# Performance work log

Hardware: AMD Instinct MI355X
Metric: run time of the kernel (lower is better)

## Reference

```python
import jax, jax.numpy as jnp
import numpy as np

FP16_MIN = -65504.0
FP16_MAX = 65504.0

B, S, D, H = 2, 2048, 1024, 16
HD = D // H


def setup_inputs() -> dict:
    key = jax.random.key(0)
    ks = jax.random.split(key, 12)
    s = 0.02
    inp = {
        "x_q": jax.random.normal(ks[0], (B, S, D), jnp.float32),
        "x_k": jax.random.normal(ks[1], (B, S, D), jnp.float32),
        "x_v": jax.random.normal(ks[2], (B, S, D), jnp.float32),
        # causal mask [B, 1, S, S]; 0 entries are masked out
        "mask": jnp.broadcast_to(jnp.tril(jnp.ones((S, S), jnp.int32)), (B, 1, S, S)),
        "Wq": jax.random.normal(ks[3], (D, D), jnp.float32) * s,
        "bq": jnp.zeros((D,), jnp.float32),
        "Wk": jax.random.normal(ks[4], (D, D), jnp.float32) * s,
        "bk": jnp.zeros((D,), jnp.float32),
        "Wv": jax.random.normal(ks[5], (D, D), jnp.float32) * s,
        "bv": jnp.zeros((D,), jnp.float32),
        "Wo": jax.random.normal(ks[6], (D, D), jnp.float32) * s,
        "bo": jnp.zeros((D,), jnp.float32),
    }
    return inp


def _split_heads(x):
    # [B, S, D] -> [B, H, S, HD]
    b, s, _ = x.shape
    return x.reshape(b, s, H, HD).transpose(0, 2, 1, 3)


def reference(x_q, x_k, x_v, mask, Wq, bq, Wk, bk, Wv, bv, Wo, bo):
    scale = jnp.sqrt(jnp.float32(HD))
    q = _split_heads(x_q @ Wq + bq)  # [B,H,S,HD]
    k = _split_heads(x_k @ Wk + bk)
    v = _split_heads(x_v @ Wv + bv)

    scores = jnp.einsum("bhqd,bhkd->bhqk", q, k) / scale  # [B,H,S,S]
    scores = jnp.where(mask == 0, FP16_MIN, scores)
    scores = jnp.where(jnp.isneginf(scores), FP16_MIN, scores)
    scores = jnp.where(jnp.isposinf(scores), FP16_MAX, scores)

    probs = jax.nn.softmax(scores, axis=-1)  # dropout p=0.0 -> identity
    ctx = jnp.einsum("bhqk,bhkd->bhqd", probs, v)  # [B,H,S,HD]
    ctx = ctx.transpose(0, 2, 1, 3).reshape(x_q.shape[0], x_q.shape[1], D)
    out = ctx @ Wo + bo
    return out, probs
```

## Files before the change

kernel.cpp:

```cpp
#include <hip/hip_runtime.h>


typedef __bf16 bf16x8 __attribute__((ext_vector_type(8)));
typedef float f32x4 __attribute__((ext_vector_type(4)));

__device__ __forceinline__ unsigned short f2bf(float f) {
  unsigned int u = __builtin_bit_cast(unsigned int, f);
  u += 0x7fffu + ((u >> 16) & 1u);
  return (unsigned short)(u >> 16);
}
__device__ __forceinline__ float bf2f_lo(unsigned int u) {
  return __builtin_bit_cast(float, u << 16);
}
__device__ __forceinline__ float bf2f_hi(unsigned int u) {
  return __builtin_bit_cast(float, u & 0xffff0000u);
}

__global__ void transpose_w(const float* __restrict__ W0, const float* __restrict__ W1,
                            const float* __restrict__ W2, const float* __restrict__ W3,
                            unsigned short* __restrict__ Wt) {
  __shared__ float t[32][33];
  const int z = blockIdx.z;
  const float* W = (z == 0) ? W0 : (z == 1) ? W1 : (z == 2) ? W2 : W3;
  unsigned short* o = Wt + (size_t)z * 1048576u;
  const int n0 = blockIdx.x * 32, k0 = blockIdx.y * 32;
  const int tx = threadIdx.x, ty = threadIdx.y;
#pragma unroll
  for (int i = 0; i < 4; i++)
    t[ty + 8 * i][tx] = W[(size_t)(k0 + ty + 8 * i) * 1024 + n0 + tx];
  __syncthreads();
#pragma unroll
  for (int i = 0; i < 4; i++)
    o[(size_t)(n0 + ty + 8 * i) * 1024 + k0 + tx] = f2bf(t[tx][ty + 8 * i]);
}

__global__ __launch_bounds__(256) void gemm_kernel(
    const void* __restrict__ A0, const void* __restrict__ A1, const void* __restrict__ A2,
    const unsigned short* __restrict__ Wtb,
    const float* __restrict__ b0, const float* __restrict__ b1, const float* __restrict__ b2,
    void* __restrict__ O0, void* __restrict__ O1, void* __restrict__ O2,
    const int mode0) {
  __shared__ unsigned short Alds[128 * 40];
  const int z = blockIdx.z;
  const int mode = mode0 + z;
  const void* Av = (z == 0) ? A0 : (z == 1) ? A1 : A2;
  const float* bias = (z == 0) ? b0 : (z == 1) ? b1 : b2;
  void* outv = (z == 0) ? O0 : (z == 1) ? O1 : O2;
  const unsigned short* Wt = Wtb + (size_t)z * 1048576u;

  const int tid = threadIdx.x;
  const int lane = tid & 63;
  const int wave = tid >> 6;
  const int wm = wave >> 1, wn = wave & 1;
  const int m0 = blockIdx.y * 128, n0 = blockIdx.x * 128;
  const int g = lane >> 4, c = lane & 15;

  f32x4 acc[4][4];
#pragma unroll
  for (int i = 0; i < 4; i++)
#pragma unroll
    for (int j = 0; j < 4; j++) acc[i][j] = (f32x4){0.f, 0.f, 0.f, 0.f};

  const int srow = tid >> 1;
  const int sch = (tid & 1) * 16;

  for (int kb = 0; kb < 1024; kb += 32) {
    if (mode < 3) {
      const float* A = (const float*)Av;
      const float4* src = (const float4*)(A + (size_t)(m0 + srow) * 1024 + kb + sch);
      unsigned int pk[8];
#pragma unroll
      for (int i = 0; i < 4; i++) {
        float4 v = src[i];
        pk[2 * i]     = (unsigned int)f2bf(v.x) | ((unsigned int)f2bf(v.y) << 16);
        pk[2 * i + 1] = (unsigned int)f2bf(v.z) | ((unsigned int)f2bf(v.w) << 16);
      }
      uint4* dst = (uint4*)&Alds[srow * 40 + sch];
      dst[0] = make_uint4(pk[0], pk[1], pk[2], pk[3]);
      dst[1] = make_uint4(pk[4], pk[5], pk[6], pk[7]);
    } else {
      const unsigned short* A = (const unsigned short*)Av;
      const uint4* src = (const uint4*)(A + (size_t)(m0 + srow) * 1024 + kb + sch);
      uint4* dst = (uint4*)&Alds[srow * 40 + sch];
      dst[0] = src[0];
      dst[1] = src[1];
    }
    __syncthreads();

    bf16x8 af[4], bfr[4];
#pragma unroll
    for (int mi = 0; mi < 4; mi++)
      af[mi] = *(const bf16x8*)&Alds[(wm * 64 + mi * 16 + c) * 40 + g * 8];
#pragma unroll
    for (int nf = 0; nf < 4; nf++)
      bfr[nf] = *(const bf16x8*)(Wt + (size_t)(n0 + wn * 64 + nf * 16 + c) * 1024 + kb + g * 8);
#pragma unroll
    for (int mi = 0; mi < 4; mi++)
#pragma unroll
      for (int nf = 0; nf < 4; nf++)
        acc[mi][nf] = __builtin_amdgcn_mfma_f32_16x16x32_bf16(af[mi], bfr[nf], acc[mi][nf], 0, 0, 0);
    __syncthreads();
  }

#pragma unroll
  for (int nf = 0; nf < 4; nf++) {
    const int col = n0 + wn * 64 + nf * 16 + c;
    const float bc = bias[col];
#pragma unroll
    for (int mi = 0; mi < 4; mi++) {
#pragma unroll
      for (int r = 0; r < 4; r++) {
        const int row = m0 + wm * 64 + mi * 16 + g * 4 + r;
        const float v = acc[mi][nf][r] + bc;
        if (mode == 0) {
          ((unsigned short*)outv)[(size_t)row * 1024 + col] = f2bf(v * 0.125f);
        } else if (mode == 1) {
          ((unsigned short*)outv)[(size_t)row * 1024 + col] = f2bf(v);
        } else if (mode == 2) {
          const int bb = row >> 11, s = row & 2047;
          ((unsigned short*)outv)[((size_t)(bb * 1024 + col)) * 2048 + s] = f2bf(v);
        } else {
          ((float*)outv)[(size_t)row * 1024 + col] = v;
        }
      }
    }
  }
}

__global__ __launch_bounds__(256) void attn_kernel(
    const unsigned short* __restrict__ Q, const unsigned short* __restrict__ K,
    const unsigned short* __restrict__ Vt, float* __restrict__ probs,
    unsigned short* __restrict__ ctx) {
  __shared__ unsigned short Klds[64 * 72];
  __shared__ unsigned short Vlds[64 * 72];
  __shared__ unsigned short Plds[64 * 72];

  const int tid = threadIdx.x;
  const int lane = tid & 63, wave = tid >> 6;
  const int g = lane >> 4, c = lane & 15;
  const int q0 = blockIdx.x * 64;
  const int h = blockIdx.y, b = blockIdx.z;
  const int qrow0 = q0 + wave * 16;

  const unsigned short* Qh = Q + ((size_t)(b * 2048 + qrow0)) * 1024 + h * 64;
  const unsigned short* Kh = K + ((size_t)b * 2048) * 1024 + h * 64;
  const unsigned short* Vh = Vt + ((size_t)(b * 16 + h)) * 64 * 2048;
  float* Ph = probs + ((size_t)((b * 16 + h) * 2048 + q0)) * 2048;

  const bf16x8 qa0 = *(const bf16x8*)&Qh[(size_t)c * 1024 + g * 8];
  const bf16x8 qa1 = *(const bf16x8*)&Qh[(size_t)c * 1024 + 32 + g * 8];

  const int srow = tid >> 2;
  const int scol = (tid & 3) * 16;
  const int kb_end = q0 + 64;

#define QK_TILE()                                                                        \
  f32x4 sv[4];                                                                           \
  _Pragma("unroll")                                                                      \
  for (int sub = 0; sub < 4; sub++) {                                                    \
    sv[sub] = (f32x4){0.f, 0.f, 0.f, 0.f};                                               \
    const unsigned short* Kr = &Klds[(sub * 16 + c) * 72];                               \
    sv[sub] = __builtin_amdgcn_mfma_f32_16x16x32_bf16(qa0, *(const bf16x8*)&Kr[g * 8], sv[sub], 0, 0, 0); \
    sv[sub] = __builtin_amdgcn_mfma_f32_16x16x32_bf16(qa1, *(const bf16x8*)&Kr[32 + g * 8], sv[sub], 0, 0, 0); \
  }                                                                                      \
  if (kb + 63 > qrow0) {                                                                 \
    _Pragma("unroll")                                                                    \
    for (int sub = 0; sub < 4; sub++)                                                    \
      _Pragma("unroll")                                                                  \
      for (int r = 0; r < 4; r++)                                                        \
        if (kb + sub * 16 + c > qrow0 + g * 4 + r) sv[sub][r] = -1e30f;                  \
  }

  float lp[4] = {0.f, 0.f, 0.f, 0.f};
  for (int kb = 0; kb < kb_end; kb += 64) {
    {
      const uint4* ksrc = (const uint4*)(Kh + (size_t)(kb + srow) * 1024 + scol);
      uint4* kdst = (uint4*)&Klds[srow * 72 + scol];
      kdst[0] = ksrc[0];
      kdst[1] = ksrc[1];
    }
    __syncthreads();
    QK_TILE();
#pragma unroll
    for (int r = 0; r < 4; r++)
      lp[r] += __expf(sv[0][r]) + __expf(sv[1][r]) + __expf(sv[2][r]) + __expf(sv[3][r]);
    __syncthreads();
  }
#pragma unroll
  for (int off = 1; off < 16; off <<= 1)
#pragma unroll
    for (int r = 0; r < 4; r++) lp[r] += __shfl_xor(lp[r], off);
  float invl[4];
#pragma unroll
  for (int r = 0; r < 4; r++) invl[r] = 1.0f / lp[r];

  f32x4 cacc[4];
#pragma unroll
  for (int nf = 0; nf < 4; nf++) cacc[nf] = (f32x4){0.f, 0.f, 0.f, 0.f};

  for (int kb = 0; kb < kb_end; kb += 64) {
    {
      const uint4* ksrc = (const uint4*)(Kh + (size_t)(kb + srow) * 1024 + scol);
      uint4* kdst = (uint4*)&Klds[srow * 72 + scol];
      kdst[0] = ksrc[0];
      kdst[1] = ksrc[1];
      const uint4* vsrc = (const uint4*)(Vh + (size_t)srow * 2048 + kb + scol);
      uint4* vdst = (uint4*)&Vlds[srow * 72 + scol];
      vdst[0] = vsrc[0];
      vdst[1] = vsrc[1];
    }
    __syncthreads();
    QK_TILE();
#pragma unroll
    for (int sub = 0; sub < 4; sub++)
#pragma unroll
      for (int r = 0; r < 4; r++) {
        const float p = __expf(sv[sub][r]) * invl[r];
        Plds[(wave * 16 + g * 4 + r) * 72 + sub * 16 + c] = f2bf(p);
      }
    const bf16x8 pa0 = *(const bf16x8*)&Plds[(wave * 16 + c) * 72 + g * 8];
    const bf16x8 pa1 = *(const bf16x8*)&Plds[(wave * 16 + c) * 72 + 32 + g * 8];
#pragma unroll
    for (int nf = 0; nf < 4; nf++) {
      const bf16x8 vf0 = *(const bf16x8*)&Vlds[(nf * 16 + c) * 72 + g * 8];
      const bf16x8 vf1 = *(const bf16x8*)&Vlds[(nf * 16 + c) * 72 + 32 + g * 8];
      cacc[nf] = __builtin_amdgcn_mfma_f32_16x16x32_bf16(pa0, vf0, cacc[nf], 0, 0, 0);
      cacc[nf] = __builtin_amdgcn_mfma_f32_16x16x32_bf16(pa1, vf1, cacc[nf], 0, 0, 0);
    }
    __syncthreads();
    {
      const int row = tid >> 2;
      const int cb = (tid & 3) * 16;
      const uint4* ps = (const uint4*)&Plds[row * 72 + cb];
      const uint4 a = ps[0], bb4 = ps[1];
      float* dst = Ph + (size_t)row * 2048 + kb + cb;
      ((float4*)dst)[0] = make_float4(bf2f_lo(a.x), bf2f_hi(a.x), bf2f_lo(a.y), bf2f_hi(a.y));
      ((float4*)dst)[1] = make_float4(bf2f_lo(a.z), bf2f_hi(a.z), bf2f_lo(a.w), bf2f_hi(a.w));
      ((float4*)dst)[2] = make_float4(bf2f_lo(bb4.x), bf2f_hi(bb4.x), bf2f_lo(bb4.y), bf2f_hi(bb4.y));
      ((float4*)dst)[3] = make_float4(bf2f_lo(bb4.z), bf2f_hi(bb4.z), bf2f_lo(bb4.w), bf2f_hi(bb4.w));
    }
  }
#undef QK_TILE

#pragma unroll
  for (int nf = 0; nf < 4; nf++)
#pragma unroll
    for (int r = 0; r < 4; r++)
      ctx[((size_t)(b * 2048 + qrow0 + g * 4 + r)) * 1024 + h * 64 + nf * 16 + c] =
          f2bf(cacc[nf][r]);

  if (kb_end < 2048) {
    const float4 zz = make_float4(0.f, 0.f, 0.f, 0.f);
    for (int row = 0; row < 64; ++row) {
      float* pr = Ph + (size_t)row * 2048;
      for (int col = kb_end + tid * 4; col < 2048; col += 1024)
        *(float4*)&pr[col] = zz;
    }
  }
}

extern "C" void kernel_launch(void* const* d_in, const int* in_sizes, int n_in,
                              void* d_out, int out_size, void* d_ws, size_t ws_size,
                              hipStream_t stream) {
  if (ws_size < (size_t)40 * 1024 * 1024) return;

  const float* xq = (const float*)d_in[0];
  const float* xk = (const float*)d_in[1];
  const float* xv = (const float*)d_in[2];
  const float* Wq = (const float*)d_in[4];
  const float* bq = (const float*)d_in[5];
  const float* Wk = (const float*)d_in[6];
  const float* bk = (const float*)d_in[7];
  const float* Wv = (const float*)d_in[8];
  const float* bv = (const float*)d_in[9];
  const float* Wo = (const float*)d_in[10];
  const float* bo = (const float*)d_in[11];

  unsigned short* ws = (unsigned short*)d_ws;
  unsigned short* Wt = ws;
  unsigned short* Qw = ws + (size_t)4 * 1048576u;
  unsigned short* Kw = Qw + 4194304u;
  unsigned short* Vtw = Kw + 4194304u;
  unsigned short* Cw = Vtw + 4194304u;

  float* out = (float*)d_out;
  float* probs = out + 4194304u;

  transpose_w<<<dim3(32, 32, 4), dim3(32, 8), 0, stream>>>(Wq, Wk, Wv, Wo, Wt);
  gemm_kernel<<<dim3(8, 32, 3), 256, 0, stream>>>(xq, xk, xv, Wt, bq, bk, bv,
                                                  Qw, Kw, Vtw, 0);
  attn_kernel<<<dim3(32, 16, 2), 256, 0, stream>>>(Qw, Kw, Vtw, probs, Cw);
  gemm_kernel<<<dim3(8, 32, 1), 256, 0, stream>>>(Cw, Cw, Cw, Wt + 3u * 1048576u,
                                                  bo, bo, bo, out, out, out, 3);
}
```

Before: 391.8 us.

## Halve GEMM M-tile with register prefetch; enlarge attention block to 128 queries

The GEMM now uses 64-row M tiles, so twice as many blocks are launched, and it prefetches the next K-slice of A into registers while the current slice is computed. The attention kernel moves to 512-thread blocks covering 128 query rows, which halves redundant K/V tile loads per query. It also register-prefetches the next K/V tiles, and waves past the causal diagonal skip compute and only write zero probabilities. In exchange, GEMM reuse of the weight reads drops and the attention blocks use more registers and LDS, which can reduce occupancy. The larger blocks also worsen load imbalance across the causal grid.

```diff
diff --git a/kernel.cpp b/kernel.cpp
--- a/kernel.cpp
+++ b/kernel.cpp
@@ -40,7 +40,7 @@
     const float* __restrict__ b0, const float* __restrict__ b1, const float* __restrict__ b2,
     void* __restrict__ O0, void* __restrict__ O1, void* __restrict__ O2,
     const int mode0) {
-  __shared__ unsigned short Alds[128 * 40];
+  __shared__ unsigned short Alds[64 * 40];
   const int z = blockIdx.z;
   const int mode = mode0 + z;
   const void* Av = (z == 0) ? A0 : (z == 1) ? A1 : A2;
@@ -52,65 +52,64 @@
   const int lane = tid & 63;
   const int wave = tid >> 6;
   const int wm = wave >> 1, wn = wave & 1;
-  const int m0 = blockIdx.y * 128, n0 = blockIdx.x * 128;
+  const int m0 = blockIdx.y * 64, n0 = blockIdx.x * 128;
   const int g = lane >> 4, c = lane & 15;
 
-  f32x4 acc[4][4];
-#pragma unroll
-  for (int i = 0; i < 4; i++)
+  f32x4 acc[2][4];
+#pragma unroll
+  for (int i = 0; i < 2; i++)
 #pragma unroll
     for (int j = 0; j < 4; j++) acc[i][j] = (f32x4){0.f, 0.f, 0.f, 0.f};
 
-  const int srow = tid >> 1;
-  const int sch = (tid & 1) * 16;
-
+  const int srow = tid >> 2;
+  const int sch = (tid & 3) * 8;
+
+#define LOAD_PACK(KB, DST)                                                        \
+  if (mode < 3) {                                                                 \
+    const float* A = (const float*)Av;                                            \
+    const float4* src = (const float4*)(A + (size_t)(m0 + srow) * 1024 + (KB) + sch); \
+    const float4 v0 = src[0], v1 = src[1];                                        \
+    DST.x = (unsigned int)f2bf(v0.x) | ((unsigned int)f2bf(v0.y) << 16);          \
+    DST.y = (unsigned int)f2bf(v0.z) | ((unsigned int)f2bf(v0.w) << 16);          \
+    DST.z = (unsigned int)f2bf(v1.x) | ((unsigned int)f2bf(v1.y) << 16);          \
+    DST.w = (unsigned int)f2bf(v1.z) | ((unsigned int)f2bf(v1.w) << 16);          \
+  } else {                                                                        \
+    const unsigned short* A = (const unsigned short*)Av;                          \
+    DST = *(const uint4*)(A + (size_t)(m0 + srow) * 1024 + (KB) + sch);           \
+  }
+
+  uint4 pk;
+  LOAD_PACK(0, pk);
   for (int kb = 0; kb < 1024; kb += 32) {
-    if (mode < 3) {
-      const float* A = (const float*)Av;
-      const float4* src = (const float4*)(A + (size_t)(m0 + srow) * 1024 + kb + sch);
-      unsigned int pk[8];
-#pragma unroll
-      for (int i = 0; i < 4; i++) {
-        float4 v = src[i];
-        pk[2 * i]     = (unsigned int)f2bf(v.x) | ((unsigned int)f2bf(v.y) << 16);
-        pk[2 * i + 1] = (unsigned int)f2bf(v.z) | ((unsigned int)f2bf(v.w) << 16);
-      }
-      uint4* dst = (uint4*)&Alds[srow * 40 + sch];
-      dst[0] = make_uint4(pk[0], pk[1], pk[2], pk[3]);
-      dst[1] = make_uint4(pk[4], pk[5], pk[6], pk[7]);
-    } else {
-      const unsigned short* A = (const unsigned short*)Av;
-      const uint4* src = (const uint4*)(A + (size_t)(m0 + srow) * 1024 + kb + sch);
-      uint4* dst = (uint4*)&Alds[srow * 40 + sch];
-      dst[0] = src[0];
-      dst[1] = src[1];
-    }
+    *(uint4*)&Alds[srow * 40 + sch] = pk;
+    if (kb + 32 < 1024) { LOAD_PACK(kb + 32, pk); }
     __syncthreads();
 
-    bf16x8 af[4], bfr[4];
-#pragma unroll
-    for (int mi = 0; mi < 4; mi++)
-      af[mi] = *(const bf16x8*)&Alds[(wm * 64 + mi * 16 + c) * 40 + g * 8];
+    bf16x8 af[2], bfr[4];
+#pragma unroll
+    for (int mi = 0; mi < 2; mi++)
+      af[mi] = *(const bf16x8*)&Alds[(wm * 32 + mi * 16 + c) * 40 + g * 8];
 #pragma unroll
     for (int nf = 0; nf < 4; nf++)
       bfr[nf] = *(const bf16x8*)(Wt + (size_t)(n0 + wn * 64 + nf * 16 + c) * 1024 + kb + g * 8);
 #pragma unroll
-    for (int mi = 0; mi < 4; mi++)
+    for (int mi = 0; mi < 2; mi++)
 #pragma unroll
       for (int nf = 0; nf < 4; nf++)
         acc[mi][nf] = __builtin_amdgcn_mfma_f32_16x16x32_bf16(af[mi], bfr[nf], acc[mi][nf], 0, 0, 0);
     __syncthreads();
   }
+#undef LOAD_PACK
 
 #pragma unroll
   for (int nf = 0; nf < 4; nf++) {
     const int col = n0 + wn * 64 + nf * 16 + c;
     const float bc = bias[col];
 #pragma unroll
-    for (int mi = 0; mi < 4; mi++) {
+    for (int mi = 0; mi < 2; mi++) {
 #pragma unroll
       for (int r = 0; r < 4; r++) {
-        const int row = m0 + wm * 64 + mi * 16 + g * 4 + r;
+        const int row = m0 + wm * 32 + mi * 16 + g * 4 + r;
         const float v = acc[mi][nf][r] + bc;
         if (mode == 0) {
           ((unsigned short*)outv)[(size_t)row * 1024 + col] = f2bf(v * 0.125f);
@@ -127,32 +126,34 @@
   }
 }
 
-__global__ __launch_bounds__(256) void attn_kernel(
+__global__ __launch_bounds__(512, 4) void attn_kernel(
     const unsigned short* __restrict__ Q, const unsigned short* __restrict__ K,
     const unsigned short* __restrict__ Vt, float* __restrict__ probs,
     unsigned short* __restrict__ ctx) {
   __shared__ unsigned short Klds[64 * 72];
   __shared__ unsigned short Vlds[64 * 72];
-  __shared__ unsigned short Plds[64 * 72];
+  __shared__ unsigned short Plds[128 * 72];
 
   const int tid = threadIdx.x;
   const int lane = tid & 63, wave = tid >> 6;
   const int g = lane >> 4, c = lane & 15;
-  const int q0 = blockIdx.x * 64;
-  const int h = blockIdx.y, b = blockIdx.z;
+  const int bh = blockIdx.x;
+  const int b = bh >> 4, h = bh & 15;
+  const int q0 = blockIdx.y * 128;
   const int qrow0 = q0 + wave * 16;
+  const int wave_kend = qrow0 + 16;
 
   const unsigned short* Qh = Q + ((size_t)(b * 2048 + qrow0)) * 1024 + h * 64;
   const unsigned short* Kh = K + ((size_t)b * 2048) * 1024 + h * 64;
-  const unsigned short* Vh = Vt + ((size_t)(b * 16 + h)) * 64 * 2048;
-  float* Ph = probs + ((size_t)((b * 16 + h) * 2048 + q0)) * 2048;
+  const unsigned short* Vh = Vt + ((size_t)bh) * 64 * 2048;
+  float* Ph = probs + ((size_t)(bh * 2048 + q0)) * 2048;
 
   const bf16x8 qa0 = *(const bf16x8*)&Qh[(size_t)c * 1024 + g * 8];
   const bf16x8 qa1 = *(const bf16x8*)&Qh[(size_t)c * 1024 + 32 + g * 8];
 
-  const int srow = tid >> 2;
-  const int scol = (tid & 3) * 16;
-  const int kb_end = q0 + 64;
+  const int srow = tid >> 3;
+  const int scol = (tid & 7) * 8;
+  const int kb_end = q0 + 128;
 
 #define QK_TILE()                                                                        \
   f32x4 sv[4];                                                                           \
@@ -172,19 +173,21 @@
   }
 
   float lp[4] = {0.f, 0.f, 0.f, 0.f};
-  for (int kb = 0; kb < kb_end; kb += 64) {
-    {
-      const uint4* ksrc = (const uint4*)(Kh + (size_t)(kb + srow) * 1024 + scol);
-      uint4* kdst = (uint4*)&Klds[srow * 72 + scol];
-      kdst[0] = ksrc[0];
-      kdst[1] = ksrc[1];
+  {
+    uint4 kreg = *(const uint4*)(Kh + (size_t)srow * 1024 + scol);
+    for (int kb = 0; kb < kb_end; kb += 64) {
+      *(uint4*)&Klds[srow * 72 + scol] = kreg;
+      if (kb + 64 < kb_end)
+        kreg = *(const uint4*)(Kh + (size_t)(kb + 64 + srow) * 1024 + scol);
+      __syncthreads();
+      if (kb < wave_kend) {
+        QK_TILE();
+#pragma unroll
+        for (int r = 0; r < 4; r++)
+          lp[r] += __expf(sv[0][r]) + __expf(sv[1][r]) + __expf(sv[2][r]) + __expf(sv[3][r]);
+      }
+      __syncthreads();
     }
-    __syncthreads();
-    QK_TILE();
-#pragma unroll
-    for (int r = 0; r < 4; r++)
-      lp[r] += __expf(sv[0][r]) + __expf(sv[1][r]) + __expf(sv[2][r]) + __expf(sv[3][r]);
-    __syncthreads();
   }
 #pragma unroll
   for (int off = 1; off < 16; off <<= 1)
@@ -198,46 +201,54 @@
 #pragma unroll
   for (int nf = 0; nf < 4; nf++) cacc[nf] = (f32x4){0.f, 0.f, 0.f, 0.f};
 
-  for (int kb = 0; kb < kb_end; kb += 64) {
-    {
-      const uint4* ksrc = (const uint4*)(Kh + (size_t)(kb + srow) * 1024 + scol);
-      uint4* kdst = (uint4*)&Klds[srow * 72 + scol];
-      kdst[0] = ksrc[0];
-      kdst[1] = ksrc[1];
-      const uint4* vsrc = (const uint4*)(Vh + (size_t)srow * 2048 + kb + scol);
-      uint4* vdst = (uint4*)&Vlds[srow * 72 + scol];
-      vdst[0] = vsrc[0];
-      vdst[1] = vsrc[1];
-    }
-    __syncthreads();
-    QK_TILE();
-#pragma unroll
-    for (int sub = 0; sub < 4; sub++)
-#pragma unroll
-      for (int r = 0; r < 4; r++) {
-        const float p = __expf(sv[sub][r]) * invl[r];
-        Plds[(wave * 16 + g * 4 + r) * 72 + sub * 16 + c] = f2bf(p);
-      }
-    const bf16x8 pa0 = *(const bf16x8*)&Plds[(wave * 16 + c) * 72 + g * 8];
-    const bf16x8 pa1 = *(const bf16x8*)&Plds[(wave * 16 + c) * 72 + 32 + g * 8];
-#pragma unroll
-    for (int nf = 0; nf < 4; nf++) {
-      const bf16x8 vf0 = *(const bf16x8*)&Vlds[(nf * 16 + c) * 72 + g * 8];
-      const bf16x8 vf1 = *(const bf16x8*)&Vlds[(nf * 16 + c) * 72 + 32 + g * 8];
-      cacc[nf] = __builtin_amdgcn_mfma_f32_16x16x32_bf16(pa0, vf0, cacc[nf], 0, 0, 0);
-      cacc[nf] = __builtin_amdgcn_mfma_f32_16x16x32_bf16(pa1, vf1, cacc[nf], 0, 0, 0);
-    }
-    __syncthreads();
-    {
-      const int row = tid >> 2;
-      const int cb = (tid & 3) * 16;
-      const uint4* ps = (const uint4*)&Plds[row * 72 + cb];
-      const uint4 a = ps[0], bb4 = ps[1];
-      float* dst = Ph + (size_t)row * 2048 + kb + cb;
-      ((float4*)dst)[0] = make_float4(bf2f_lo(a.x), bf2f_hi(a.x), bf2f_lo(a.y), bf2f_hi(a.y));
-      ((float4*)dst)[1] = make_float4(bf2f_lo(a.z), bf2f_hi(a.z), bf2f_lo(a.w), bf2f_hi(a.w));
-      ((float4*)dst)[2] = make_float4(bf2f_lo(bb4.x), bf2f_hi(bb4.x), bf2f_lo(bb4.y), bf2f_hi(bb4.y));
-      ((float4*)dst)[3] = make_float4(bf2f_lo(bb4.z), bf2f_hi(bb4.z), bf2f_lo(bb4.w), bf2f_hi(bb4.w));
+  {
+    uint4 kreg = *(const uint4*)(Kh + (size_t)srow * 1024 + scol);
+    uint4 vreg = *(const uint4*)(Vh + (size_t)srow * 2048 + scol);
+    for (int kb = 0; kb < kb_end; kb += 64) {
+      *(uint4*)&Klds[srow * 72 + scol] = kreg;
+      *(uint4*)&Vlds[srow * 72 + scol] = vreg;
+      if (kb + 64 < kb_end) {
+        kreg = *(const uint4*)(Kh + (size_t)(kb + 64 + srow) * 1024 + scol);
+        vreg = *(const uint4*)(Vh + (size_t)srow * 2048 + kb + 64 + scol);
+      }
+      __syncthreads();
+      if (kb < wave_kend) {
+        QK_TILE();
+#pragma unroll
+        for (int sub = 0; sub < 4; sub++)
+#pragma unroll
+          for (int r = 0; r < 4; r++) {
+            const float p = __expf(sv[sub][r]) * invl[r];
+            Plds[(wave * 16 + g * 4 + r) * 72 + sub * 16 + c] = f2bf(p);
+          }
+        const bf16x8 pa0 = *(const bf16x8*)&Plds[(wave * 16 + c) * 72 + g * 8];
+        const bf16x8 pa1 = *(const bf16x8*)&Plds[(wave * 16 + c) * 72 + 32 + g * 8];
+#pragma unroll
+        for (int nf = 0; nf < 4; nf++) {
+          const bf16x8 vf0 = *(const bf16x8*)&Vlds[(nf * 16 + c) * 72 + g * 8];
+          const bf16x8 vf1 = *(const bf16x8*)&Vlds[(nf * 16 + c) * 72 + 32 + g * 8];
+          cacc[nf] = __builtin_amdgcn_mfma_f32_16x16x32_bf16(pa0, vf0, cacc[nf], 0, 0, 0);
+          cacc[nf] = __builtin_amdgcn_mfma_f32_16x16x32_bf16(pa1, vf1, cacc[nf], 0, 0, 0);
+        }
+      } else {
+#pragma unroll
+        for (int sub = 0; sub < 4; sub++)
+#pragma unroll
+          for (int r = 0; r < 4; r++)
+            Plds[(wave * 16 + g * 4 + r) * 72 + sub * 16 + c] = 0;
+      }
+      __syncthreads();
+      {
+        const int prow = tid >> 2;
+        const int pcb = (tid & 3) * 16;
+        const uint4* ps = (const uint4*)&Plds[prow * 72 + pcb];
+        const uint4 a = ps[0], b4 = ps[1];
+        float* dst = Ph + (size_t)prow * 2048 + kb + pcb;
+        ((float4*)dst)[0] = make_float4(bf2f_lo(a.x), bf2f_hi(a.x), bf2f_lo(a.y), bf2f_hi(a.y));
+        ((float4*)dst)[1] = make_float4(bf2f_lo(a.z), bf2f_hi(a.z), bf2f_lo(a.w), bf2f_hi(a.w));
+        ((float4*)dst)[2] = make_float4(bf2f_lo(b4.x), bf2f_hi(b4.x), bf2f_lo(b4.y), bf2f_hi(b4.y));
+        ((float4*)dst)[3] = make_float4(bf2f_lo(b4.z), bf2f_hi(b4.z), bf2f_lo(b4.w), bf2f_hi(b4.w));
+      }
     }
   }
 #undef QK_TILE
@@ -251,10 +262,10 @@
 
   if (kb_end < 2048) {
     const float4 zz = make_float4(0.f, 0.f, 0.f, 0.f);
-    for (int row = 0; row < 64; ++row) {
+    for (int row = 0; row < 128; ++row) {
       float* pr = Ph + (size_t)row * 2048;
-      for (int col = kb_end + tid * 4; col < 2048; col += 1024)
-        *(float4*)&pr[col] = zz;
+      const int col = kb_end + tid * 4;
+      if (col < 2048) *(float4*)&pr[col] = zz;
     }
   }
 }
@@ -287,9 +298,9 @@
   float* probs = out + 4194304u;
 
   transpose_w<<<dim3(32, 32, 4), dim3(32, 8), 0, stream>>>(Wq, Wk, Wv, Wo, Wt);
-  gemm_kernel<<<dim3(8, 32, 3), 256, 0, stream>>>(xq, xk, xv, Wt, bq, bk, bv,
+  gemm_kernel<<<dim3(8, 64, 3), 256, 0, stream>>>(xq, xk, xv, Wt, bq, bk, bv,
                                                   Qw, Kw, Vtw, 0);
-  attn_kernel<<<dim3(32, 16, 2), 256, 0, stream>>>(Qw, Kw, Vtw, probs, Cw);
-  gemm_kernel<<<dim3(8, 32, 1), 256, 0, stream>>>(Cw, Cw, Cw, Wt + 3u * 1048576u,
+  attn_kernel<<<dim3(32, 16, 1), 512, 0, stream>>>(Qw, Kw, Vtw, probs, Cw);
+  gemm_kernel<<<dim3(8, 64, 1), 256, 0, stream>>>(Cw, Cw, Cw, Wt + 3u * 1048576u,
                                                   bo, bo, bo, out, out, out, 3);
 }
```

Measured after the change: 366.2 us. -6.5%, faster.
